# Kernel tuning notes

Hardware: AMD Instinct MI355X
Metric: run time of the kernel (lower is better)

## Reference

```python
import jax, jax.numpy as jnp
import numpy as np

V, H, B, NS, SL, QL, AL = 100000, 256, 64, 40, 30, 20, 12
NUM_EPISODE = 3


def setup_inputs() -> dict:
    key = jax.random.key(0)
    ks = iter(jax.random.split(key, 48))
    def p(shape, scale=0.05):
        return jax.random.normal(next(ks), shape, jnp.float32) * scale
    d = {}
    d["c_p"] = jax.random.randint(next(ks), (B, NS, SL), 0, V, dtype=jnp.int32)
    d["c_mask"] = jnp.zeros((B, NS, SL), jnp.int32)
    d["q_p"] = jax.random.randint(next(ks), (B, QL), 0, V, dtype=jnp.int32)
    d["q_mask"] = jnp.zeros((B, QL), jnp.int32)
    d["a_I_p"] = jax.random.randint(next(ks), (B, AL), 0, V, dtype=jnp.int32)
    d["a_I_mask"] = jnp.zeros((B, AL), jnp.int32)
    d["a_II_p"] = jax.random.randint(next(ks), (B, AL), 0, V, dtype=jnp.int32)
    d["a_II_mask"] = jnp.zeros((B, AL), jnp.int32)
    d["embed"] = p((V, H)).at[0].set(0.0)  # padding_idx=0
    for name in ["ctx", "q", "ans", "attn", "mem"]:
        d[name + "_Wih"] = p((3 * H, H))
        d[name + "_Whh"] = p((3 * H, H))
        d[name + "_bih"] = p((3 * H,))
        d[name + "_bhh"] = p((3 * H,))
    d["gate_W1"] = p((H, 7 * H)); d["gate_b1"] = p((H,))
    d["gate_W2"] = p((1, H));     d["gate_b2"] = p((1,))
    d["out_W1"] = p((H, 3 * H)); d["out_b1"] = p((H,))
    d["out_W2"] = p((2, H));     d["out_b2"] = p((2,))
    return d


def _gru_step(h, gi_t, Whh, bhh):
    # PyTorch GRU cell math; gates ordered (r, z, n)
    gh = h @ Whh.T + bhh
    i_r, i_z, i_n = jnp.split(gi_t, 3, -1)
    h_r, h_z, h_n = jnp.split(gh, 3, -1)
    r = jax.nn.sigmoid(i_r + h_r)
    z = jax.nn.sigmoid(i_z + h_z)
    n = jnp.tanh(i_n + r * h_n)
    return (1.0 - z) * n + z * h


def _run_gru(x, Wih, Whh, bih, bhh):
    # x: [N, T, H] -> outputs [N, T, H], zero initial hidden
    gi = jnp.einsum('nth,gh->ntg', x, Wih) + bih  # precompute input projections
    h0 = jnp.zeros((x.shape[0], Whh.shape[1]), x.dtype)
    def step(h, g_t):
        h2 = _gru_step(h, g_t, Whh, bhh)
        return h2, h2
    _, outs = jax.lax.scan(step, h0, jnp.swapaxes(gi, 0, 1))
    return jnp.swapaxes(outs, 0, 1)


def _gather_last(outs, mask):
    # real_length = number of zeros in mask (0 marks a valid token)
    lengths = jnp.sum(mask == 0, axis=-1)
    idx = jnp.clip(lengths - 1, 0, outs.shape[1] - 1)
    return jnp.take_along_axis(outs, idx[:, None, None], axis=1)[:, 0]


def _forward(c_p, c_mask, q_p, q_mask, a_I_p, a_I_mask, a_II_p, a_II_mask,
             embed,
             ctx_Wih, ctx_Whh, ctx_bih, ctx_bhh,
             q_Wih, q_Whh, q_bih, q_bhh,
             ans_Wih, ans_Whh, ans_bih, ans_bhh,
             attn_Wih, attn_Whh, attn_bih, attn_bhh,
             mem_Wih, mem_Whh, mem_bih, mem_bhh,
             gate_W1, gate_b1, gate_W2, gate_b2,
             out_W1, out_b1, out_W2, out_b2):
    b, ns, sl = c_p.shape
    # Context encoding: all (batch, sentence) pairs through one batched GRU
    ce = embed[c_p.reshape(b * ns, sl)]                      # [B*NS, SL, H]
    c_out = _run_gru(ce, ctx_Wih, ctx_Whh, ctx_bih, ctx_bhh)
    enc_ctx = _gather_last(c_out, c_mask.reshape(b * ns, sl)).reshape(b, ns, -1)  # [B, NS, H]
    # Question / answers
    enc_q = _gather_last(_run_gru(embed[q_p], q_Wih, q_Whh, q_bih, q_bhh), q_mask)          # [B, H]
    enc_a1 = _gather_last(_run_gru(embed[a_I_p], ans_Wih, ans_Whh, ans_bih, ans_bhh), a_I_mask)
    enc_a2 = _gather_last(_run_gru(embed[a_II_p], ans_Wih, ans_Whh, ans_bih, ans_bhh), a_II_mask)
    # Episodic memory: gated attention GRU scan over context sentences
    ctx_t = jnp.swapaxes(enc_ctx, 0, 1)  # [NS, B, H]
    memory = enc_q
    for _ in range(NUM_EPISODE):
        mem_now = memory
        def step(h, ct):
            feat = jnp.concatenate([ct, mem_now, enc_q, ct * enc_q, ct * mem_now,
                                    jnp.abs(ct - enc_q), jnp.abs(ct - mem_now)], axis=1)  # [B, 7H]
            g = jax.nn.sigmoid(jnp.tanh(feat @ gate_W1.T + gate_b1) @ gate_W2.T + gate_b2)  # [B, 1]
            hc = _gru_step(h, ct @ attn_Wih.T + attn_bih, attn_Whh, attn_bhh)
            return g * hc + (1.0 - g) * h, None
        e, _ = jax.lax.scan(step, jnp.zeros_like(memory), ctx_t)
        memory = _gru_step(memory, e @ mem_Wih.T + mem_bih, mem_Whh, mem_bhh)
    final = jnp.concatenate([memory, enc_a1, enc_a2], axis=1)  # [B, 3H]
    logits = jnp.tanh(final @ out_W1.T + out_b1) @ out_W2.T + out_b2  # [B, 2]
    return jax.nn.softmax(logits, axis=-1)


def reference(c_p, c_mask, q_p, q_mask, a_I_p, a_I_mask, a_II_p, a_II_mask,
              embed,
              ctx_Wih, ctx_Whh, ctx_bih, ctx_bhh,
              q_Wih, q_Whh, q_bih, q_bhh,
              ans_Wih, ans_Whh, ans_bih, ans_bhh,
              attn_Wih, attn_Whh, attn_bih, attn_bhh,
              mem_Wih, mem_Whh, mem_bih, mem_bhh,
              gate_W1, gate_b1, gate_W2, gate_b2,
              out_W1, out_b1, out_W2, out_b2):
    return _forward(c_p, c_mask, q_p, q_mask, a_I_p, a_I_mask, a_II_p, a_II_mask,
                    embed,
                    ctx_Wih, ctx_Whh, ctx_bih, ctx_bhh,
                    q_Wih, q_Whh, q_bih, q_bhh,
                    ans_Wih, ans_Whh, ans_bih, ans_bhh,
                    attn_Wih, attn_Whh, attn_bih, attn_bhh,
                    mem_Wih, mem_Whh, mem_bih, mem_bhh,
                    gate_W1, gate_b1, gate_W2, gate_b2,
                    out_W1, out_b1, out_W2, out_b2)
```

## Files before the change

### kernel.cpp

```cpp
#include <hip/hip_runtime.h>

typedef unsigned short u16;
typedef __bf16 bf16x8 __attribute__((ext_vector_type(8)));
typedef float f32x4 __attribute__((ext_vector_type(4)));

#define NSENT 40
#define SLEN 30
#define QLEN 20
#define ALEN 12
#define SCTX 2560

__device__ __forceinline__ float b2f(u16 u){ union{float f; unsigned i;} v; v.i = ((unsigned)u)<<16; return v.f; }
__device__ __forceinline__ u16 f2b(float f){ union{float f; unsigned u;} v; v.f=f; unsigned u=v.u; u += ((u>>16)&1u) + 0x7fffu; return (u16)(u>>16); }
__device__ __forceinline__ float sigm(float x){ return __builtin_amdgcn_rcpf(1.f + __expf(-x)); }
__device__ __forceinline__ float tanh_(float x){
  float a = fminf(fmaxf(2.f*x, -30.f), 30.f);
  float e = __expf(a);
  return 1.f - 2.f*__builtin_amdgcn_rcpf(e + 1.f);
}
__device__ __forceinline__ f32x4 mfma16(bf16x8 a, bf16x8 b, f32x4 c){
  return __builtin_amdgcn_mfma_f32_16x16x32_bf16(a, b, c, 0, 0, 0);
}

__global__ void k_prep(
    const float* cWih, const float* cWhh, const float* qWih, const float* qWhh,
    const float* aWih, const float* aWhh, const float* tWih, const float* tWhh,
    const float* mWih, const float* mWhh, const float* gW1,
    const float* cbih, const float* cbhh, const float* qbih, const float* qbhh,
    const float* abih, const float* abhh, const float* tbih, const float* tbhh,
    u16* P0,u16* P1,u16* P2,u16* P3,u16* P4,u16* P5,u16* P6,u16* P7,
    u16* PmWih, u16* PmWhh, u16* PgW1,
    float* B0,float* B1,float* B2,float* B3,float* B4,float* B5,float* B6,float* B7)
{
  int i = blockIdx.x*512 + threadIdx.x;
  if (i < 1572864){
    int seg = i/196608; int e = i - seg*196608;
    int np = e>>8, k = e&255;
    int g16 = np/48, rem = np - g16*48, gate = rem>>4, cc = rem&15;
    int j = gate*256 + g16*16 + cc;
    const float* S;
    u16* D;
    switch(seg){
      case 0: S=cWih; D=P0; break; case 1: S=cWhh; D=P1; break;
      case 2: S=qWih; D=P2; break; case 3: S=qWhh; D=P3; break;
      case 4: S=aWih; D=P4; break; case 5: S=aWhh; D=P5; break;
      case 6: S=tWih; D=P6; break; default: S=tWhh; D=P7; break;
    }
    D[e] = f2b(S[j*256 + k]);
  } else if (i < 1966080){
    int e = i - 1572864;
    if (e < 196608) PmWih[e]=f2b(mWih[e]);
    else PmWhh[e-196608]=f2b(mWhh[e-196608]);
  } else if (i < 2424832){
    int e = i - 1966080;
    PgW1[e] = f2b(gW1[e]);
  } else {
    int e = i - 2424832;
    int seg = e/768; int np = e - seg*768;
    int g16 = np/48, rem = np - g16*48, gate = rem>>4, cc = rem&15;
    int j = gate*256 + g16*16 + cc;
    const float* S; float* D;
    switch(seg){
      case 0: S=cbih; D=B0; break; case 1: S=cbhh; D=B1; break;
      case 2: S=qbih; D=B2; break; case 3: S=qbhh; D=B3; break;
      case 4: S=abih; D=B4; break; case 5: S=abhh; D=B5; break;
      case 6: S=tbih; D=B6; break; default: S=tbhh; D=B7; break;
    }
    D[np] = S[j];
  }
}

__global__ __launch_bounds__(512, 2) void k_xproj(
    const int* c_p, const int* q_p, const int* a1p, const int* a2p,
    const float* embed,
    const u16* cWihP, const u16* qWihP, const u16* aWihP,
    const float* cBih, const float* qBih, const float* aBih,
    u16* gi_c, u16* gi_q, u16* gi_a1, u16* gi_a2)
{
  __shared__ u16 xb[32][264];
  __shared__ u16 go[32][776];
  int bid=blockIdx.x, tid=threadIdx.x;
  const int* toks; const u16* W; const float* bias; u16* out; int rl;
  if (bid < 2400){ toks=c_p; W=cWihP; bias=cBih; out=gi_c; rl=bid*32; }
  else if (bid < 2440){ toks=q_p; W=qWihP; bias=qBih; out=gi_q; rl=(bid-2400)*32; }
  else if (bid < 2464){ toks=a1p; W=aWihP; bias=aBih; out=gi_a1; rl=(bid-2440)*32; }
  else               { toks=a2p; W=aWihP; bias=aBih; out=gi_a2; rl=(bid-2464)*32; }
  #pragma unroll
  for (int p=0;p<4;p++){
    int i=p*512+tid; int row=i>>6, f4=i&63;
    int tok = toks[rl+row];
    float4 v = *((const float4*)(embed + (long)tok*256) + f4);
    u16* dst = &xb[row][f4*4];
    dst[0]=f2b(v.x); dst[1]=f2b(v.y); dst[2]=f2b(v.z); dst[3]=f2b(v.w);
  }
  const int w=tid>>6, lane=tid&63, c=lane&15, quad=lane>>4;
  f32x4 acc[2][6];
  #pragma unroll
  for (int Mt=0;Mt<2;Mt++)
    #pragma unroll
    for (int nt=0;nt<6;nt++) acc[Mt][nt]=(f32x4){0.f,0.f,0.f,0.f};
  __syncthreads();
  #pragma unroll
  for (int Kt=0;Kt<8;Kt++){
    bf16x8 a0 = *(const bf16x8*)&xb[c][Kt*32+quad*8];
    bf16x8 a1 = *(const bf16x8*)&xb[16+c][Kt*32+quad*8];
    #pragma unroll
    for (int nt=0;nt<6;nt++){
      bf16x8 bfr = *(const bf16x8*)(cWihP==W||qWihP==W||aWihP==W ?
                    W + ((w*6+nt)*16+c)*256 + Kt*32 + quad*8 :
                    W + ((w*6+nt)*16+c)*256 + Kt*32 + quad*8);
      acc[0][nt]=mfma16(a0,bfr,acc[0][nt]);
      acc[1][nt]=mfma16(a1,bfr,acc[1][nt]);
    }
  }
  float biasv[6];
  #pragma unroll
  for (int nt=0;nt<6;nt++) biasv[nt]=bias[(w*6+nt)*16+c];
  #pragma unroll
  for (int Mt=0;Mt<2;Mt++)
    #pragma unroll
    for (int nt=0;nt<6;nt++)
      #pragma unroll
      for (int r=0;r<4;r++)
        go[Mt*16+quad*4+r][(w*6+nt)*16+c]=f2b(acc[Mt][nt][r]+biasv[nt]);
  __syncthreads();
  #pragma unroll
  for (int p=0;p<6;p++){
    int idx=p*512+tid;
    int row=idx/96, ch=idx-row*96;
    *(uint4*)(out + (long)(rl+row)*768 + ch*8) = *(uint4*)((char*)&go[row][0] + ch*16);
  }
}

__global__ __launch_bounds__(512, 2) void k_enc_scan(
    const int* c_mask, const int* q_mask, const int* a1m, const int* a2m,
    const u16* cWhhP, const u16* qWhhP, const u16* aWhhP,
    const float* cBhh, const float* qBhh, const float* aBhh,
    const u16* gi_c, const u16* gi_q, const u16* gi_a1, const u16* gi_a2,
    u16* enc_hi, u16* enc_lo, float* enc_qf, float* enc_a1f, float* enc_a2f)
{
  __shared__ u16 hhi[16][264];
  __shared__ u16 hlo[16][264];
  __shared__ u16 gib[2][16][768];
  __shared__ int idxs[16];
  int bid=blockIdx.x, tid=threadIdx.x;
  const int* msk; const u16* W; const float* bhh; const u16* gi; int T, seq0, mode;
  u16 *ohi=0, *olo=0; float* of=0;
  if (bid<160){ msk=c_mask; W=cWhhP; bhh=cBhh; gi=gi_c; T=SLEN; seq0=bid*16; mode=0; ohi=enc_hi; olo=enc_lo; }
  else if (bid<164){ msk=q_mask; W=qWhhP; bhh=qBhh; gi=gi_q; T=QLEN; seq0=(bid-160)*16; mode=1; of=enc_qf; }
  else if (bid<168){ msk=a1m; W=aWhhP; bhh=aBhh; gi=gi_a1; T=ALEN; seq0=(bid-164)*16; mode=1; of=enc_a1f; }
  else             { msk=a2m; W=aWhhP; bhh=aBhh; gi=gi_a2; T=ALEN; seq0=(bid-168)*16; mode=1; of=enc_a2f; }
  if (tid<16){
    int len=0; const int* mr=msk+(seq0+tid)*T;
    for (int t=0;t<T;t++) len += (mr[t]==0);
    int id=len-1; if(id<0)id=0; if(id>T-1)id=T-1; idxs[tid]=id;
  }
  for (int i=tid;i<16*264;i+=512){ ((u16*)hhi)[i]=0; ((u16*)hlo)[i]=0; }
  const int w=tid>>6, lane=tid&63, c=lane&15, quad=lane>>4;
  float biasv[6];
  #pragma unroll
  for (int nt=0;nt<6;nt++) biasv[nt]=bhh[w*96+nt*16+c];
  uint4 breg[48];
  #pragma unroll
  for (int nt=0;nt<6;nt++)
    #pragma unroll
    for (int Kt=0;Kt<8;Kt++)
      breg[nt*8+Kt] = *(const uint4*)(W + (w*96+nt*16+c)*256 + Kt*32 + quad*8);
  float hreg[8];
  #pragma unroll
  for (int i=0;i<8;i++) hreg[i]=0.f;
  const u16* gp[3];
  #pragma unroll
  for (int p=0;p<3;p++){
    int idx=p*512+tid; int row=idx/96, ch=idx-row*96;
    gp[p] = gi + ((long)(seq0+row)*T)*768 + ch*8;
  }
  u16* gf0 = &gib[0][0][0];
  u16* gf1 = &gib[1][0][0];
  {
    uint4 s0[3];
    #pragma unroll
    for (int p=0;p<3;p++) s0[p]=*(const uint4*)(gp[p]);
    #pragma unroll
    for (int p=0;p<3;p++) *(uint4*)(gf0 + (p*512+tid)*8) = s0[p];
  }
  __syncthreads();
  int cbuf=0;
  for (int t=0;t<T;t++){
    uint4 pre[3];
    bool pf = (t+1<T);
    if (pf){
      #pragma unroll
      for (int p=0;p<3;p++) pre[p]=*(const uint4*)(gp[p]+(long)(t+1)*768);
    }
    f32x4 acc[6];
    #pragma unroll
    for (int nt=0;nt<6;nt++) acc[nt]=(f32x4){0.f,0.f,0.f,0.f};
    #pragma unroll
    for (int Kt=0;Kt<8;Kt++){
      bf16x8 a=*(const bf16x8*)&hhi[c][Kt*32+quad*8];
      #pragma unroll
      for (int nt=0;nt<6;nt++) acc[nt]=mfma16(a,*(const bf16x8*)&breg[nt*8+Kt],acc[nt]);
    }
    #pragma unroll
    for (int Kt=0;Kt<8;Kt++){
      bf16x8 a=*(const bf16x8*)&hlo[c][Kt*32+quad*8];
      #pragma unroll
      for (int nt=0;nt<6;nt++) acc[nt]=mfma16(a,*(const bf16x8*)&breg[nt*8+Kt],acc[nt]);
    }
    if (pf){
      u16* gs = cbuf ? gf0 : gf1;
      #pragma unroll
      for (int p=0;p<3;p++) *(uint4*)(gs + (p*512+tid)*8) = pre[p];
    }
    const u16* gb = cbuf ? gf1 : gf0;
    #pragma unroll
    for (int r=0;r<4;r++){
      int m = quad*4+r;
      const u16* gr = gb + m*768 + w*96 + c;
      #pragma unroll
      for (int jj=0;jj<2;jj++){
        int j = w*32+jj*16+c;
        float ir = b2f(gr[jj*48]);
        float iz = b2f(gr[jj*48+16]);
        float in_= b2f(gr[jj*48+32]);
        float hr = acc[jj*3+0][r]+biasv[jj*3+0];
        float hz = acc[jj*3+1][r]+biasv[jj*3+1];
        float hn = acc[jj*3+2][r]+biasv[jj*3+2];
        float rr=sigm(ir+hr), zz=sigm(iz+hz), nn=tanh_(in_+rr*hn);
        float ho=hreg[r*2+jj];
        float hnew=(1.f-zz)*nn+zz*ho;
        hreg[r*2+jj]=hnew;
        u16 hi_=f2b(hnew); u16 lo_=f2b(hnew-b2f(hi_));
        hhi[m][j]=hi_; hlo[m][j]=lo_;
        if (t==idxs[m]){
          long o=(long)(seq0+m)*256+j;
          if (mode==0){ ohi[o]=hi_; olo[o]=lo_; }
          else of[o]=hnew;
        }
      }
    }
    __syncthreads();
    cbuf^=1;
  }
}

__global__ __launch_bounds__(512, 2) void k_gi(
    const u16* enc_hi, const u16* enc_lo, const u16* tWihP, const float* tBih,
    float* gi_attn, const float* enc_qf, float* mem_f)
{
  int bid=blockIdx.x, tid=threadIdx.x;
  if (bid==40){ for (int i=tid;i<64*256;i+=512) mem_f[i]=enc_qf[i]; return; }
  __shared__ u16 ahi[64][264];
  __shared__ u16 alo[64][264];
  int seq0=bid*64;
  #pragma unroll
  for (int p=0;p<4;p++){
    int i=p*512+tid; int row=i>>5, ch=i&31;
    *(uint4*)((char*)&ahi[row][0]+ch*16) = *((const uint4*)(enc_hi+(long)(seq0+row)*256)+ch);
    *(uint4*)((char*)&alo[row][0]+ch*16) = *((const uint4*)(enc_lo+(long)(seq0+row)*256)+ch);
  }
  const int w=tid>>6, lane=tid&63, c=lane&15, quad=lane>>4;
  f32x4 acc[4][6];
  #pragma unroll
  for (int Mt=0;Mt<4;Mt++)
    #pragma unroll
    for (int nt=0;nt<6;nt++) acc[Mt][nt]=(f32x4){0.f,0.f,0.f,0.f};
  __syncthreads();
  #pragma unroll
  for (int Kt=0;Kt<8;Kt++){
    bf16x8 a[4];
    #pragma unroll
    for (int Mt=0;Mt<4;Mt++) a[Mt]=*(const bf16x8*)&ahi[Mt*16+c][Kt*32+quad*8];
    #pragma unroll
    for (int nt=0;nt<6;nt++){
      bf16x8 bfr=*(const bf16x8*)(tWihP + ((w*6+nt)*16+c)*256 + Kt*32 + quad*8);
      #pragma unroll
      for (int Mt=0;Mt<4;Mt++) acc[Mt][nt]=mfma16(a[Mt],bfr,acc[Mt][nt]);
    }
  }
  #pragma unroll
  for (int Kt=0;Kt<8;Kt++){
    bf16x8 a[4];
    #pragma unroll
    for (int Mt=0;Mt<4;Mt++) a[Mt]=*(const bf16x8*)&alo[Mt*16+c][Kt*32+quad*8];
    #pragma unroll
    for (int nt=0;nt<6;nt++){
      bf16x8 bfr=*(const bf16x8*)(tWihP + ((w*6+nt)*16+c)*256 + Kt*32 + quad*8);
      #pragma unroll
      for (int Mt=0;Mt<4;Mt++) acc[Mt][nt]=mfma16(a[Mt],bfr,acc[Mt][nt]);
    }
  }
  #pragma unroll
  for (int nt=0;nt<6;nt++){
    float bv=tBih[(w*6+nt)*16+c];
    #pragma unroll
    for (int Mt=0;Mt<4;Mt++)
      #pragma unroll
      for (int r=0;r<4;r++)
        gi_attn[(long)(seq0+Mt*16+quad*4+r)*768 + (w*6+nt)*16+c] = acc[Mt][nt][r]+bv;
  }
}

__global__ __launch_bounds__(512, 1) void k_gatepre(
    const u16* enc_hi, const u16* enc_lo, const float* enc_qf,
    const u16* W1, const float* b1, float* partial)
{
  __shared__ float ctf[32][257];
  __shared__ float qvf[32][257];
  __shared__ u16 ab[32][264];
  int bid=blockIdx.x, tid=threadIdx.x, seq0=bid*32;
  #pragma unroll
  for (int p=0;p<16;p++){
    int i=p*512+tid; int row=i>>8, j=i&255;
    int grow=seq0+row; int b=grow/NSENT;
    ctf[row][j]=b2f(enc_hi[(long)grow*256+j])+b2f(enc_lo[(long)grow*256+j]);
    qvf[row][j]=enc_qf[b*256+j];
  }
  const int w=tid>>6, lane=tid&63, c=lane&15, quad=lane>>4;
  f32x4 acc[2][2];
  #pragma unroll
  for (int nt=0;nt<2;nt++){
    float bv=b1[(w*2+nt)*16+c];
// ... 103 lines not shown
    for (int nt=0;nt<2;nt++) s += tanh_(acc[Mt][nt][r])*w2v[nt];
    pm[i]=s;
  }
  #pragma unroll
  for (int off=1;off<16;off<<=1)
    #pragma unroll
    for (int i=0;i<8;i++) pm[i]+=__shfl_xor(pm[i],off,64);
  if (c==0){
    #pragma unroll
    for (int i=0;i<8;i++){ int m=(i>>2)*16+quad*4+(i&3); pl[m][w]=pm[i]; }
  }
  __syncthreads();
  if (tid<32){
    float s=b2v[0];
    #pragma unroll
    for (int ww=0;ww<8;ww++) s+=pl[tid][ww];
    g[seq0+tid]=sigm(s);
  }
}

__global__ __launch_bounds__(512, 2) void k_scan(
    const u16* tWhhP, const float* tBhh,
    const float* gi_attn, const float* g,
    float* mem_f, const u16* mWihB, const u16* mWhhB,
    const float* mbih, const float* mbhh)
{
  __shared__ u16 hb[16][264];
  __shared__ u16 mhi[16][264];
  __shared__ u16 mlo[16][264];
  __shared__ float gia[2][3072];
  __shared__ float gl[4][40];
  __shared__ float gh[4][772];
  __shared__ float gh2[4][772];
  __shared__ float memfl[4][256];
  int bid=blockIdx.x, tid=threadIdx.x, b0=bid*4;
  const int w=tid>>6, lane=tid&63, c=lane&15, quad=lane>>4;
  for (int i=tid;i<16*264;i+=512){ ((u16*)hb)[i]=0; ((u16*)mhi)[i]=0; ((u16*)mlo)[i]=0; }
  for (int i=tid;i<1024;i+=512){
    int m=i>>8, j=i&255;
    float v=mem_f[(b0+m)*256+j]; memfl[m][j]=v;
    u16 hi_=f2b(v); mhi[m][j]=hi_; mlo[m][j]=f2b(v-b2f(hi_));
  }
  if (tid<160){ int m=tid/40, s=tid-m*40; gl[m][s]=g[(b0+m)*40+s]; }
  float biasv[6];
  #pragma unroll
  for (int nt=0;nt<6;nt++) biasv[nt]=tBhh[w*96+nt*16+c];
  uint4 breg[48];
  #pragma unroll
  for (int nt=0;nt<6;nt++)
    #pragma unroll
    for (int Kt=0;Kt<8;Kt++)
      breg[nt*8+Kt] = *(const uint4*)(tWhhP + (w*96+nt*16+c)*256 + Kt*32 + quad*8);
  float hreg[8];
  #pragma unroll
  for (int i=0;i<8;i++) hreg[i]=0.f;
  int i4a = tid, i4b = 512+tid;
  int ma = i4a/192, ca=(i4a-ma*192)*4;
  int mb = i4b/192, cb=(i4b-mb*192)*4;
  const float* gpa = gi_attn + ((long)(b0+ma)*40)*768 + ca;
  const float* gpb = gi_attn + ((long)(b0+mb)*40)*768 + cb;
  {
    float4 v0=*(const float4*)(gpa);
    *(float4*)&gia[0][i4a*4]=v0;
    if (tid<256){ float4 v1=*(const float4*)(gpb); *(float4*)&gia[0][i4b*4]=v1; }
  }
  __syncthreads();
  int cbuf=0;
  for (int s=0;s<NSENT;s++){
    float4 p0, p1;
    bool pf=(s+1<NSENT);
    if (pf){
      p0=*(const float4*)(gpa + (long)(s+1)*768);
      if (tid<256) p1=*(const float4*)(gpb + (long)(s+1)*768);
    }
    f32x4 acc[6];
    #pragma unroll
    for (int nt=0;nt<6;nt++) acc[nt]=(f32x4){0.f,0.f,0.f,0.f};
    #pragma unroll
    for (int Kt=0;Kt<8;Kt++){
      bf16x8 a=*(const bf16x8*)&hb[c][Kt*32+quad*8];
      #pragma unroll
      for (int nt=0;nt<6;nt++) acc[nt]=mfma16(a,*(const bf16x8*)&breg[nt*8+Kt],acc[nt]);
    }
    if (pf){
      float* gs=&gia[1^cbuf][0];
      *(float4*)(gs+i4a*4)=p0;
      if (tid<256) *(float4*)(gs+i4b*4)=p1;
    }
    if (quad==0){
      const float* ga=&gia[cbuf][0];
      #pragma unroll
      for (int r=0;r<4;r++){
        float gv = gl[r][s];
        const float* gr = ga + r*768 + w*96 + c;
        #pragma unroll
        for (int jj=0;jj<2;jj++){
          int j = w*32+jj*16+c;
          float ir = gr[jj*48];
          float iz = gr[jj*48+16];
          float in_= gr[jj*48+32];
          float hr = acc[jj*3+0][r]+biasv[jj*3+0];
          float hz = acc[jj*3+1][r]+biasv[jj*3+1];
          float hn = acc[jj*3+2][r]+biasv[jj*3+2];
          float rr=sigm(ir+hr), zz=sigm(iz+hz), nn=tanh_(in_+rr*hn);
          float ho=hreg[r*2+jj];
          float hc=(1.f-zz)*nn+zz*ho;
          float hnew=gv*hc+(1.f-gv)*ho;
          hreg[r*2+jj]=hnew;
          hb[r][j]=f2b(hnew);
        }
      }
    }
    __syncthreads();
    cbuf^=1;
  }
  f32x4 ai[6], ah[6];
  #pragma unroll
  for (int nt=0;nt<6;nt++){ ai[nt]=(f32x4){0.f,0.f,0.f,0.f}; ah[nt]=ai[nt]; }
  #pragma unroll
  for (int Kt=0;Kt<8;Kt++){
    bf16x8 a=*(const bf16x8*)&hb[c][Kt*32+quad*8];
    #pragma unroll
    for (int nt=0;nt<6;nt++){
      bf16x8 bfr=*(const bf16x8*)(mWihB + ((w*6+nt)*16+c)*256 + Kt*32 + quad*8);
      ai[nt]=mfma16(a,bfr,ai[nt]);
    }
  }
  #pragma unroll
  for (int Kt=0;Kt<8;Kt++){
    bf16x8 a=*(const bf16x8*)&mhi[c][Kt*32+quad*8];
    #pragma unroll
    for (int nt=0;nt<6;nt++){
      bf16x8 bfr=*(const bf16x8*)(mWhhB + ((w*6+nt)*16+c)*256 + Kt*32 + quad*8);
      ah[nt]=mfma16(a,bfr,ah[nt]);
    }
  }
  #pragma unroll
  for (int Kt=0;Kt<8;Kt++){
    bf16x8 a=*(const bf16x8*)&mlo[c][Kt*32+quad*8];
    #pragma unroll
    for (int nt=0;nt<6;nt++){
      bf16x8 bfr=*(const bf16x8*)(mWhhB + ((w*6+nt)*16+c)*256 + Kt*32 + quad*8);
      ah[nt]=mfma16(a,bfr,ah[nt]);
    }
  }
  if (quad==0){
    #pragma unroll
    for (int nt=0;nt<6;nt++)
      #pragma unroll
      for (int r=0;r<4;r++){
        gh[r][(w*6+nt)*16+c]=ai[nt][r];
        gh2[r][(w*6+nt)*16+c]=ah[nt][r];
      }
  }
  __syncthreads();
  #pragma unroll
  for (int p=0;p<2;p++){
    int uid=p*512+tid; int m=uid>>8, j=uid&255;
    float ir=gh[m][j]+mbih[j], iz=gh[m][256+j]+mbih[256+j], in_=gh[m][512+j]+mbih[512+j];
    float hr=gh2[m][j]+mbhh[j], hz=gh2[m][256+j]+mbhh[256+j], hn=gh2[m][512+j]+mbhh[512+j];
    float rr=sigm(ir+hr), zz=sigm(iz+hz), nn=tanh_(in_+rr*hn);
    float mo=memfl[m][j];
    mem_f[(b0+m)*256+j]=(1.f-zz)*nn+zz*mo;
  }
}

__global__ void k_final(const float* mem_f, const float* a1f, const float* a2f,
    const float* W1o, const float* b1o, const float* W2o, const float* b2o, float* outp)
{
  __shared__ float af[768];
  __shared__ float tl[256];
  __shared__ float lg[2];
  int b=blockIdx.x, tid=threadIdx.x;
  af[tid]     = mem_f[b*256+tid];
  af[256+tid] = a1f[b*256+tid];
  af[512+tid] = a2f[b*256+tid];
  __syncthreads();
  float s=b1o[tid];
  const float* wr=W1o + (long)tid*768;
  for (int k=0;k<768;k++) s += af[k]*wr[k];
  tl[tid]=tanh_(s);
  __syncthreads();
  if (tid<2){
    float l=b2o[tid];
    const float* w2=W2o + tid*256;
    for (int k=0;k<256;k++) l += tl[k]*w2[k];
// ... 10 lines not shown

extern "C" void kernel_launch(void* const* d_in, const int* in_sizes, int n_in,
                              void* d_out, int out_size, void* d_ws, size_t ws_size,
                              hipStream_t stream) {
  const int* c_p   = (const int*)d_in[0];
  const int* c_m   = (const int*)d_in[1];
  const int* q_p   = (const int*)d_in[2];
  const int* q_m   = (const int*)d_in[3];
  const int* a1p   = (const int*)d_in[4];
  const int* a1m   = (const int*)d_in[5];
  const int* a2p   = (const int*)d_in[6];
  const int* a2m   = (const int*)d_in[7];
  const float* embed = (const float*)d_in[8];
  const float* cWih=(const float*)d_in[9],  *cWhh=(const float*)d_in[10], *cbih=(const float*)d_in[11], *cbhh=(const float*)d_in[12];
  const float* qWih=(const float*)d_in[13], *qWhh=(const float*)d_in[14], *qbih=(const float*)d_in[15], *qbhh=(const float*)d_in[16];
  const float* aWih=(const float*)d_in[17], *aWhh=(const float*)d_in[18], *abih=(const float*)d_in[19], *abhh=(const float*)d_in[20];
  const float* tWih=(const float*)d_in[21], *tWhh=(const float*)d_in[22], *tbih=(const float*)d_in[23], *tbhh=(const float*)d_in[24];
  const float* mWih=(const float*)d_in[25], *mWhh=(const float*)d_in[26], *mbih=(const float*)d_in[27], *mbhh=(const float*)d_in[28];
  const float* gW1=(const float*)d_in[29], *gb1=(const float*)d_in[30], *gW2=(const float*)d_in[31], *gb2=(const float*)d_in[32];
  const float* oW1=(const float*)d_in[33], *ob1=(const float*)d_in[34], *oW2=(const float*)d_in[35], *ob2=(const float*)d_in[36];

  char* ws = (char*)d_ws;
  size_t off = 0;
  u16* P0=(u16*)(ws+off); off+=393216;
  u16* P1=(u16*)(ws+off); off+=393216;
  u16* P2=(u16*)(ws+off); off+=393216;
  u16* P3=(u16*)(ws+off); off+=393216;
  u16* P4=(u16*)(ws+off); off+=393216;
  u16* P5=(u16*)(ws+off); off+=393216;
  u16* P6=(u16*)(ws+off); off+=393216;
  u16* P7=(u16*)(ws+off); off+=393216;
  u16* PmWih=(u16*)(ws+off); off+=393216;
  u16* PmWhh=(u16*)(ws+off); off+=393216;
  u16* PgW1 =(u16*)(ws+off); off+=917504;
  float* B0=(float*)(ws+off); off+=3072;
  float* B1=(float*)(ws+off); off+=3072;
  float* B2=(float*)(ws+off); off+=3072;
  float* B3=(float*)(ws+off); off+=3072;
  float* B4=(float*)(ws+off); off+=3072;
  float* B5=(float*)(ws+off); off+=3072;
  float* B6=(float*)(ws+off); off+=3072;
  float* B7=(float*)(ws+off); off+=3072;
  u16* gi_c =(u16*)(ws+off); off+=(size_t)76800*768*2;
  u16* gi_q =(u16*)(ws+off); off+=(size_t)1280*768*2;
  u16* gi_a1=(u16*)(ws+off); off+=(size_t)768*768*2;
  u16* gi_a2=(u16*)(ws+off); off+=(size_t)768*768*2;
  u16* enc_hi=(u16*)(ws+off); off+=(size_t)SCTX*256*2;
  u16* enc_lo=(u16*)(ws+off); off+=(size_t)SCTX*256*2;
  float* enc_qf =(float*)(ws+off); off+=64*256*4;
  float* enc_a1f=(float*)(ws+off); off+=64*256*4;
  float* enc_a2f=(float*)(ws+off); off+=64*256*4;
  float* mem_f  =(float*)(ws+off); off+=64*256*4;
  float* gi_attn=(float*)(ws+off); off+=(size_t)SCTX*768*4;
  float* partial=(float*)(ws+off); off+=(size_t)SCTX*256*4;
  float* gbuf   =(float*)(ws+off); off+=SCTX*4;

  k_prep<<<4748, 512, 0, stream>>>(cWih,cWhh,qWih,qWhh,aWih,aWhh,tWih,tWhh,mWih,mWhh,gW1,
      cbih,cbhh,qbih,qbhh,abih,abhh,tbih,tbhh,
      P0,P1,P2,P3,P4,P5,P6,P7, PmWih,PmWhh,PgW1,
      B0,B1,B2,B3,B4,B5,B6,B7);

  k_xproj<<<2488, 512, 0, stream>>>(c_p,q_p,a1p,a2p, embed,
      P0,P2,P4, B0,B2,B4, gi_c,gi_q,gi_a1,gi_a2);

  k_enc_scan<<<172, 512, 0, stream>>>(c_m,q_m,a1m,a2m,
      P1,P3,P5, B1,B3,B5, gi_c,gi_q,gi_a1,gi_a2,
      enc_hi,enc_lo, enc_qf,enc_a1f,enc_a2f);

  k_gi<<<41, 512, 0, stream>>>(enc_hi,enc_lo, P6, B6, gi_attn, enc_qf, mem_f);

  k_gatepre<<<80, 512, 0, stream>>>(enc_hi,enc_lo, enc_qf, PgW1, gb1, partial);

  for (int ep=0; ep<3; ep++){
    k_gate<<<80, 512, 0, stream>>>(enc_hi,enc_lo, mem_f, partial, PgW1, gW2, gb2, gbuf);
    k_scan<<<16, 512, 0, stream>>>(P7, B7, gi_attn, gbuf, mem_f, PmWih, PmWhh, mbih, mbhh);
  }

  k_final<<<64, 256, 0, stream>>>(mem_f, enc_a1f, enc_a2f, oW1, ob1, oW2, ob2, (float*)d_out);
}
```

Before: 957.7 us.

## Store gate projections in per-lane fragment layout and widen attention scan tiles

The input-projection kernels now write gi in a per-lane fragment order (24 values per lane per timestep), and the scans read each lane's slice straight into registers with a register double-buffer. This removes the LDS staging buffers and an extra sync pass. The attention scan now processes 16 batch rows per block in 4 blocks instead of 4 rows in 16, so every MFMA row carries real data. The memory GRU epilogue is done in registers using permuted mem weights. The cost is that only 4 blocks run the serial attention scan, which lowers parallelism.

```diff
diff --git a/kernel.cpp b/kernel.cpp
--- a/kernel.cpp
+++ b/kernel.cpp
@@ -9,6 +9,8 @@
 #define QLEN 20
 #define ALEN 12
 #define SCTX 2560
+#define SLOT 24
+#define TP 12288
 
 __device__ __forceinline__ float b2f(u16 u){ union{float f; unsigned i;} v; v.i = ((unsigned)u)<<16; return v.f; }
 __device__ __forceinline__ u16 f2b(float f){ union{float f; unsigned u;} v; v.f=f; unsigned u=v.u; u += ((u>>16)&1u) + 0x7fffu; return (u16)(u>>16); }
@@ -28,29 +30,27 @@
     const float* mWih, const float* mWhh, const float* gW1,
     const float* cbih, const float* cbhh, const float* qbih, const float* qbhh,
     const float* abih, const float* abhh, const float* tbih, const float* tbhh,
-    u16* P0,u16* P1,u16* P2,u16* P3,u16* P4,u16* P5,u16* P6,u16* P7,
-    u16* PmWih, u16* PmWhh, u16* PgW1,
-    float* B0,float* B1,float* B2,float* B3,float* B4,float* B5,float* B6,float* B7)
+    const float* mbih, const float* mbhh,
+    u16* P0,u16* P1,u16* P2,u16* P3,u16* P4,u16* P5,u16* P6,u16* P7,u16* P8,u16* P9,
+    u16* PgW1,
+    float* B0,float* B1,float* B2,float* B3,float* B4,float* B5,float* B6,float* B7,
+    float* B8,float* B9)
 {
   int i = blockIdx.x*512 + threadIdx.x;
-  if (i < 1572864){
+  if (i < 1966080){
     int seg = i/196608; int e = i - seg*196608;
     int np = e>>8, k = e&255;
     int g16 = np/48, rem = np - g16*48, gate = rem>>4, cc = rem&15;
     int j = gate*256 + g16*16 + cc;
-    const float* S;
-    u16* D;
+    const float* S; u16* D;
     switch(seg){
       case 0: S=cWih; D=P0; break; case 1: S=cWhh; D=P1; break;
       case 2: S=qWih; D=P2; break; case 3: S=qWhh; D=P3; break;
       case 4: S=aWih; D=P4; break; case 5: S=aWhh; D=P5; break;
-      case 6: S=tWih; D=P6; break; default: S=tWhh; D=P7; break;
+      case 6: S=tWih; D=P6; break; case 7: S=tWhh; D=P7; break;
+      case 8: S=mWih; D=P8; break; default: S=mWhh; D=P9; break;
     }
     D[e] = f2b(S[j*256 + k]);
-  } else if (i < 1966080){
-    int e = i - 1572864;
-    if (e < 196608) PmWih[e]=f2b(mWih[e]);
-    else PmWhh[e-196608]=f2b(mWhh[e-196608]);
   } else if (i < 2424832){
     int e = i - 1966080;
     PgW1[e] = f2b(gW1[e]);
@@ -64,7 +64,8 @@
       case 0: S=cbih; D=B0; break; case 1: S=cbhh; D=B1; break;
       case 2: S=qbih; D=B2; break; case 3: S=qbhh; D=B3; break;
       case 4: S=abih; D=B4; break; case 5: S=abhh; D=B5; break;
-      case 6: S=tbih; D=B6; break; default: S=tbhh; D=B7; break;
+      case 6: S=tbih; D=B6; break; case 7: S=tbhh; D=B7; break;
+      case 8: S=mbih; D=B8; break; default: S=mbhh; D=B9; break;
     }
     D[np] = S[j];
   }
@@ -78,17 +79,18 @@
     u16* gi_c, u16* gi_q, u16* gi_a1, u16* gi_a2)
 {
   __shared__ u16 xb[32][264];
-  __shared__ u16 go[32][776];
   int bid=blockIdx.x, tid=threadIdx.x;
-  const int* toks; const u16* W; const float* bias; u16* out; int rl;
-  if (bid < 2400){ toks=c_p; W=cWihP; bias=cBih; out=gi_c; rl=bid*32; }
-  else if (bid < 2440){ toks=q_p; W=qWihP; bias=qBih; out=gi_q; rl=(bid-2400)*32; }
-  else if (bid < 2464){ toks=a1p; W=aWihP; bias=aBih; out=gi_a1; rl=(bid-2440)*32; }
-  else               { toks=a2p; W=aWihP; bias=aBih; out=gi_a2; rl=(bid-2464)*32; }
+  const int* toks; const u16* W; const float* bias; u16* out; int T, block, t0;
+  if (bid < 2400){ toks=c_p; W=cWihP; bias=cBih; out=gi_c; T=SLEN; block=bid/15; t0=(bid-block*15)*2; }
+  else if (bid < 2440){ int e=bid-2400; toks=q_p; W=qWihP; bias=qBih; out=gi_q; T=QLEN; block=e/10; t0=(e-block*10)*2; }
+  else if (bid < 2464){ int e=bid-2440; toks=a1p; W=aWihP; bias=aBih; out=gi_a1; T=ALEN; block=e/6; t0=(e-block*6)*2; }
+  else               { int e=bid-2464; toks=a2p; W=aWihP; bias=aBih; out=gi_a2; T=ALEN; block=e/6; t0=(e-block*6)*2; }
+  int seq0 = block*16;
   #pragma unroll
   for (int p=0;p<4;p++){
     int i=p*512+tid; int row=i>>6, f4=i&63;
-    int tok = toks[rl+row];
+    int tp=row>>4, m=row&15;
+    int tok = toks[(seq0+m)*T + t0+tp];
     float4 v = *((const float4*)(embed + (long)tok*256) + f4);
     u16* dst = &xb[row][f4*4];
     dst[0]=f2b(v.x); dst[1]=f2b(v.y); dst[2]=f2b(v.z); dst[3]=f2b(v.w);
@@ -106,29 +108,30 @@
     bf16x8 a1 = *(const bf16x8*)&xb[16+c][Kt*32+quad*8];
     #pragma unroll
     for (int nt=0;nt<6;nt++){
-      bf16x8 bfr = *(const bf16x8*)(cWihP==W||qWihP==W||aWihP==W ?
-                    W + ((w*6+nt)*16+c)*256 + Kt*32 + quad*8 :
-                    W + ((w*6+nt)*16+c)*256 + Kt*32 + quad*8);
+      bf16x8 bfr = *(const bf16x8*)(W + (w*96+nt*16+c)*256 + Kt*32 + quad*8);
       acc[0][nt]=mfma16(a0,bfr,acc[0][nt]);
       acc[1][nt]=mfma16(a1,bfr,acc[1][nt]);
     }
   }
   float biasv[6];
   #pragma unroll
-  for (int nt=0;nt<6;nt++) biasv[nt]=bias[(w*6+nt)*16+c];
-  #pragma unroll
-  for (int Mt=0;Mt<2;Mt++)
-    #pragma unroll
-    for (int nt=0;nt<6;nt++)
-      #pragma unroll
-      for (int r=0;r<4;r++)
-        go[Mt*16+quad*4+r][(w*6+nt)*16+c]=f2b(acc[Mt][nt][r]+biasv[nt]);
-  __syncthreads();
-  #pragma unroll
-  for (int p=0;p<6;p++){
-    int idx=p*512+tid;
-    int row=idx/96, ch=idx-row*96;
-    *(uint4*)(out + (long)(rl+row)*768 + ch*8) = *(uint4*)((char*)&go[row][0] + ch*16);
+  for (int nt=0;nt<6;nt++) biasv[nt]=bias[w*96+nt*16+c];
+  #pragma unroll
+  for (int tp=0;tp<2;tp++){
+    unsigned d[12];
+    #pragma unroll
+    for (int k=0;k<12;k++){
+      int i0=2*k, i1=2*k+1;
+      int r0=i0/6, re0=i0%6, jj0=re0/3, g0=re0%3;
+      int r1=i1/6, re1=i1%6, jj1=re1/3, g1=re1%3;
+      unsigned lo=f2b(acc[tp][jj0*3+g0][r0]+biasv[jj0*3+g0]);
+      unsigned hi=f2b(acc[tp][jj1*3+g1][r1]+biasv[jj1*3+g1]);
+      d[k] = lo | (hi<<16);
+    }
+    u16* dst = out + ((long)(block*T + t0+tp))*TP + (w*64+lane)*SLOT;
+    *(uint4*)(dst)    = *(uint4*)&d[0];
+    *(uint4*)(dst+8)  = *(uint4*)&d[4];
+    *(uint4*)(dst+16) = *(uint4*)&d[8];
   }
 }
 
@@ -141,15 +144,14 @@
 {
   __shared__ u16 hhi[16][264];
   __shared__ u16 hlo[16][264];
-  __shared__ u16 gib[2][16][768];
   __shared__ int idxs[16];
   int bid=blockIdx.x, tid=threadIdx.x;
   const int* msk; const u16* W; const float* bhh; const u16* gi; int T, seq0, mode;
   u16 *ohi=0, *olo=0; float* of=0;
-  if (bid<160){ msk=c_mask; W=cWhhP; bhh=cBhh; gi=gi_c; T=SLEN; seq0=bid*16; mode=0; ohi=enc_hi; olo=enc_lo; }
-  else if (bid<164){ msk=q_mask; W=qWhhP; bhh=qBhh; gi=gi_q; T=QLEN; seq0=(bid-160)*16; mode=1; of=enc_qf; }
-  else if (bid<168){ msk=a1m; W=aWhhP; bhh=aBhh; gi=gi_a1; T=ALEN; seq0=(bid-164)*16; mode=1; of=enc_a1f; }
-  else             { msk=a2m; W=aWhhP; bhh=aBhh; gi=gi_a2; T=ALEN; seq0=(bid-168)*16; mode=1; of=enc_a2f; }
+  if (bid<160){ msk=c_mask; W=cWhhP; bhh=cBhh; gi=gi_c+(long)bid*SLEN*TP; T=SLEN; seq0=bid*16; mode=0; ohi=enc_hi; olo=enc_lo; }
+  else if (bid<164){ int e=bid-160; msk=q_mask; W=qWhhP; bhh=qBhh; gi=gi_q+(long)e*QLEN*TP; T=QLEN; seq0=e*16; mode=1; of=enc_qf; }
+  else if (bid<168){ int e=bid-164; msk=a1m; W=aWhhP; bhh=aBhh; gi=gi_a1+(long)e*ALEN*TP; T=ALEN; seq0=e*16; mode=1; of=enc_a1f; }
+  else             { int e=bid-168; msk=a2m; W=aWhhP; bhh=aBhh; gi=gi_a2+(long)e*ALEN*TP; T=ALEN; seq0=e*16; mode=1; of=enc_a2f; }
   if (tid<16){
     int len=0; const int* mr=msk+(seq0+tid)*T;
     for (int t=0;t<T;t++) len += (mr[t]==0);
@@ -169,29 +171,19 @@
   float hreg[8];
   #pragma unroll
   for (int i=0;i<8;i++) hreg[i]=0.f;
-  const u16* gp[3];
-  #pragma unroll
-  for (int p=0;p<3;p++){
-    int idx=p*512+tid; int row=idx/96, ch=idx-row*96;
-    gp[p] = gi + ((long)(seq0+row)*T)*768 + ch*8;
-  }
-  u16* gf0 = &gib[0][0][0];
-  u16* gf1 = &gib[1][0][0];
-  {
-    uint4 s0[3];
-    #pragma unroll
-    for (int p=0;p<3;p++) s0[p]=*(const uint4*)(gp[p]);
-    #pragma unroll
-    for (int p=0;p<3;p++) *(uint4*)(gf0 + (p*512+tid)*8) = s0[p];
-  }
-  __syncthreads();
-  int cbuf=0;
+  const u16* gp = gi + (w*64+lane)*SLOT;
+  uint4 pA0=*(const uint4*)(gp), pA1=*(const uint4*)(gp+8), pA2=*(const uint4*)(gp+16);
+  __syncthreads();
+  int idxr[4];
+  #pragma unroll
+  for (int r=0;r<4;r++) idxr[r]=idxs[quad*4+r];
+
   for (int t=0;t<T;t++){
-    uint4 pre[3];
-    bool pf = (t+1<T);
+    uint4 pB0,pB1,pB2;
+    bool pf=(t+1<T);
     if (pf){
-      #pragma unroll
-      for (int p=0;p<3;p++) pre[p]=*(const uint4*)(gp[p]+(long)(t+1)*768);
+      const u16* gn = gp + (long)(t+1)*TP;
+      pB0=*(const uint4*)(gn); pB1=*(const uint4*)(gn+8); pB2=*(const uint4*)(gn+16);
     }
     f32x4 acc[6];
     #pragma unroll
@@ -208,32 +200,28 @@
       #pragma unroll
       for (int nt=0;nt<6;nt++) acc[nt]=mfma16(a,*(const bf16x8*)&breg[nt*8+Kt],acc[nt]);
     }
-    if (pf){
-      u16* gs = cbuf ? gf0 : gf1;
-      #pragma unroll
-      for (int p=0;p<3;p++) *(uint4*)(gs + (p*512+tid)*8) = pre[p];
-    }
-    const u16* gb = cbuf ? gf1 : gf0;
+    unsigned pd[12];
+    *(uint4*)&pd[0]=pA0; *(uint4*)&pd[4]=pA1; *(uint4*)&pd[8]=pA2;
     #pragma unroll
     for (int r=0;r<4;r++){
-      int m = quad*4+r;
-      const u16* gr = gb + m*768 + w*96 + c;
+      int m=quad*4+r;
       #pragma unroll
       for (int jj=0;jj<2;jj++){
-        int j = w*32+jj*16+c;
-        float ir = b2f(gr[jj*48]);
-        float iz = b2f(gr[jj*48+16]);
-        float in_= b2f(gr[jj*48+32]);
-        float hr = acc[jj*3+0][r]+biasv[jj*3+0];
-        float hz = acc[jj*3+1][r]+biasv[jj*3+1];
-        float hn = acc[jj*3+2][r]+biasv[jj*3+2];
+        int j=w*32+jj*16+c;
+        int ib=(r*2+jj)*3;
+        float ir = b2f((u16)((pd[ib>>1]     >> ((ib&1)*16)) & 0xffffu));
+        float iz = b2f((u16)((pd[(ib+1)>>1] >> (((ib+1)&1)*16)) & 0xffffu));
+        float in_= b2f((u16)((pd[(ib+2)>>1] >> (((ib+2)&1)*16)) & 0xffffu));
+        float hr=acc[jj*3+0][r]+biasv[jj*3+0];
+        float hz=acc[jj*3+1][r]+biasv[jj*3+1];
+        float hn=acc[jj*3+2][r]+biasv[jj*3+2];
         float rr=sigm(ir+hr), zz=sigm(iz+hz), nn=tanh_(in_+rr*hn);
         float ho=hreg[r*2+jj];
         float hnew=(1.f-zz)*nn+zz*ho;
         hreg[r*2+jj]=hnew;
         u16 hi_=f2b(hnew); u16 lo_=f2b(hnew-b2f(hi_));
         hhi[m][j]=hi_; hlo[m][j]=lo_;
-        if (t==idxs[m]){
+        if (t==idxr[r]){
           long o=(long)(seq0+m)*256+j;
           if (mode==0){ ohi[o]=hi_; olo[o]=lo_; }
           else of[o]=hnew;
@@ -241,7 +229,7 @@
       }
     }
     __syncthreads();
-    cbuf^=1;
+    pA0=pB0; pA1=pB1; pA2=pB2;
   }
 }
 
@@ -250,55 +238,53 @@
     float* gi_attn, const float* enc_qf, float* mem_f)
 {
   int bid=blockIdx.x, tid=threadIdx.x;
-  if (bid==40){ for (int i=tid;i<64*256;i+=512) mem_f[i]=enc_qf[i]; return; }
-  __shared__ u16 ahi[64][264];
-  __shared__ u16 alo[64][264];
-  int seq0=bid*64;
-  #pragma unroll
-  for (int p=0;p<4;p++){
-    int i=p*512+tid; int row=i>>5, ch=i&31;
-    *(uint4*)((char*)&ahi[row][0]+ch*16) = *((const uint4*)(enc_hi+(long)(seq0+row)*256)+ch);
-    *(uint4*)((char*)&alo[row][0]+ch*16) = *((const uint4*)(enc_lo+(long)(seq0+row)*256)+ch);
+  if (bid==160){ for (int i=tid;i<64*256;i+=512) mem_f[i]=enc_qf[i]; return; }
+  __shared__ u16 ahi[16][264];
+  __shared__ u16 alo[16][264];
+  int bblk=bid/40, s=bid-bblk*40, b0=bblk*16;
+  {
+    int row=tid>>5, ch=tid&31;
+    long seq=(long)(b0+row)*NSENT + s;
+    *(uint4*)((char*)&ahi[row][0]+ch*16) = *((const uint4*)(enc_hi+seq*256)+ch);
+    *(uint4*)((char*)&alo[row][0]+ch*16) = *((const uint4*)(enc_lo+seq*256)+ch);
   }
   const int w=tid>>6, lane=tid&63, c=lane&15, quad=lane>>4;
-  f32x4 acc[4][6];
-  #pragma unroll
-  for (int Mt=0;Mt<4;Mt++)
-    #pragma unroll
-    for (int nt=0;nt<6;nt++) acc[Mt][nt]=(f32x4){0.f,0.f,0.f,0.f};
+  f32x4 acc[6];
+  #pragma unroll
+  for (int nt=0;nt<6;nt++) acc[nt]=(f32x4){0.f,0.f,0.f,0.f};
   __syncthreads();
   #pragma unroll
   for (int Kt=0;Kt<8;Kt++){
-    bf16x8 a[4];
-    #pragma unroll
-    for (int Mt=0;Mt<4;Mt++) a[Mt]=*(const bf16x8*)&ahi[Mt*16+c][Kt*32+quad*8];
+    bf16x8 a=*(const bf16x8*)&ahi[c][Kt*32+quad*8];
     #pragma unroll
     for (int nt=0;nt<6;nt++){
-      bf16x8 bfr=*(const bf16x8*)(tWihP + ((w*6+nt)*16+c)*256 + Kt*32 + quad*8);
-      #pragma unroll
-      for (int Mt=0;Mt<4;Mt++) acc[Mt][nt]=mfma16(a[Mt],bfr,acc[Mt][nt]);
+      bf16x8 bfr=*(const bf16x8*)(tWihP + (w*96+nt*16+c)*256 + Kt*32 + quad*8);
+      acc[nt]=mfma16(a,bfr,acc[nt]);
     }
   }
   #pragma unroll
   for (int Kt=0;Kt<8;Kt++){
-    bf16x8 a[4];
-    #pragma unroll
-    for (int Mt=0;Mt<4;Mt++) a[Mt]=*(const bf16x8*)&alo[Mt*16+c][Kt*32+quad*8];
+    bf16x8 a=*(const bf16x8*)&alo[c][Kt*32+quad*8];
     #pragma unroll
     for (int nt=0;nt<6;nt++){
-      bf16x8 bfr=*(const bf16x8*)(tWihP + ((w*6+nt)*16+c)*256 + Kt*32 + quad*8);
-      #pragma unroll
-      for (int Mt=0;Mt<4;Mt++) acc[Mt][nt]=mfma16(a[Mt],bfr,acc[Mt][nt]);
-    }
-  }
-  #pragma unroll
-  for (int nt=0;nt<6;nt++){
-    float bv=tBih[(w*6+nt)*16+c];
-    #pragma unroll
-    for (int Mt=0;Mt<4;Mt++)
-      #pragma unroll
-      for (int r=0;r<4;r++)
-        gi_attn[(long)(seq0+Mt*16+quad*4+r)*768 + (w*6+nt)*16+c] = acc[Mt][nt][r]+bv;
+      bf16x8 bfr=*(const bf16x8*)(tWihP + (w*96+nt*16+c)*256 + Kt*32 + quad*8);
+      acc[nt]=mfma16(a,bfr,acc[nt]);
+    }
+  }
+  float biasv[6];
+  #pragma unroll
+  for (int nt=0;nt<6;nt++) biasv[nt]=tBih[w*96+nt*16+c];
+  float* dst = gi_attn + ((long)(bblk*40+s))*TP + (w*64+lane)*SLOT;
+  #pragma unroll
+  for (int d=0;d<6;d++){
+    float4 v;
+    #pragma unroll
+    for (int e=0;e<4;e++){
+      int idx=4*d+e;
+      int r=idx/6, rem=idx%6, jj=rem/3, g=rem%3;
+      ((float*)&v)[e]=acc[jj*3+g][r]+biasv[jj*3+g];
+    }
+    *(float4*)(dst+4*d)=v;
   }
 }
 
@@ -448,26 +434,23 @@
 __global__ __launch_bounds__(512, 2) void k_scan(
     const u16* tWhhP, const float* tBhh,
     const float* gi_attn, const float* g,
-    float* mem_f, const u16* mWihB, const u16* mWhhB,
-    const float* mbih, const float* mbhh)
+    float* mem_f, const u16* mWihP, const u16* mWhhP,
+    const float* mBih, const float* mBhh)
 {
   __shared__ u16 hb[16][264];
   __shared__ u16 mhi[16][264];
   __shared__ u16 mlo[16][264];
-  __shared__ float gia[2][3072];
-  __shared__ float gl[4][40];
-  __shared__ float gh[4][772];
-  __shared__ float gh2[4][772];
-  __shared__ float memfl[4][256];
-  int bid=blockIdx.x, tid=threadIdx.x, b0=bid*4;
+  __shared__ float memfl[16][256];
+  __shared__ float gl[16][40];
+  int bid=blockIdx.x, tid=threadIdx.x, b0=bid*16;
   const int w=tid>>6, lane=tid&63, c=lane&15, quad=lane>>4;
-  for (int i=tid;i<16*264;i+=512){ ((u16*)hb)[i]=0; ((u16*)mhi)[i]=0; ((u16*)mlo)[i]=0; }
-  for (int i=tid;i<1024;i+=512){
+  for (int i=tid;i<16*264;i+=512){ ((u16*)hb)[i]=0; }
+  for (int i=tid;i<4096;i+=512){
     int m=i>>8, j=i&255;
     float v=mem_f[(b0+m)*256+j]; memfl[m][j]=v;
     u16 hi_=f2b(v); mhi[m][j]=hi_; mlo[m][j]=f2b(v-b2f(hi_));
   }
-  if (tid<160){ int m=tid/40, s=tid-m*40; gl[m][s]=g[(b0+m)*40+s]; }
+  for (int i=tid;i<640;i+=512){ int m=i/40, s=i-m*40; gl[m][s]=g[(b0+m)*40+s]; }
   float biasv[6];
   #pragma unroll
   for (int nt=0;nt<6;nt++) biasv[nt]=tBhh[w*96+nt*16+c];
@@ -480,24 +463,19 @@
   float hreg[8];
   #pragma unroll
   for (int i=0;i<8;i++) hreg[i]=0.f;
-  int i4a = tid, i4b = 512+tid;
-  int ma = i4a/192, ca=(i4a-ma*192)*4;
-  int mb = i4b/192, cb=(i4b-mb*192)*4;
-  const float* gpa = gi_attn + ((long)(b0+ma)*40)*768 + ca;
-  const float* gpb = gi_attn + ((long)(b0+mb)*40)*768 + cb;
-  {
-    float4 v0=*(const float4*)(gpa);
-    *(float4*)&gia[0][i4a*4]=v0;
-    if (tid<256){ float4 v1=*(const float4*)(gpb); *(float4*)&gia[0][i4b*4]=v1; }
-  }
-  __syncthreads();
-  int cbuf=0;
+  const float* gp = gi_attn + ((long)bid*NSENT)*TP + (w*64+lane)*SLOT;
+  float4 pA[6];
+  #pragma unroll
+  for (int d=0;d<6;d++) pA[d]=*(const float4*)(gp+4*d);
+  __syncthreads();
+
   for (int s=0;s<NSENT;s++){
-    float4 p0, p1;
+    float4 pB[6];
     bool pf=(s+1<NSENT);
     if (pf){
-      p0=*(const float4*)(gpa + (long)(s+1)*768);
-      if (tid<256) p1=*(const float4*)(gpb + (long)(s+1)*768);
+      const float* gn = gp + (long)(s+1)*TP;
+      #pragma unroll
+      for (int d=0;d<6;d++) pB[d]=*(const float4*)(gn+4*d);
     }
     f32x4 acc[6];
     #pragma unroll
@@ -508,37 +486,30 @@
       #pragma unroll
       for (int nt=0;nt<6;nt++) acc[nt]=mfma16(a,*(const bf16x8*)&breg[nt*8+Kt],acc[nt]);
     }
-    if (pf){
-      float* gs=&gia[1^cbuf][0];
-      *(float4*)(gs+i4a*4)=p0;
-      if (tid<256) *(float4*)(gs+i4b*4)=p1;
-    }
-    if (quad==0){
-      const float* ga=&gia[cbuf][0];
-      #pragma unroll
-      for (int r=0;r<4;r++){
-        float gv = gl[r][s];
-        const float* gr = ga + r*768 + w*96 + c;
-        #pragma unroll
-        for (int jj=0;jj<2;jj++){
-          int j = w*32+jj*16+c;
-          float ir = gr[jj*48];
-          float iz = gr[jj*48+16];
-          float in_= gr[jj*48+32];
-          float hr = acc[jj*3+0][r]+biasv[jj*3+0];
-          float hz = acc[jj*3+1][r]+biasv[jj*3+1];
-          float hn = acc[jj*3+2][r]+biasv[jj*3+2];
-          float rr=sigm(ir+hr), zz=sigm(iz+hz), nn=tanh_(in_+rr*hn);
-          float ho=hreg[r*2+jj];
-          float hc=(1.f-zz)*nn+zz*ho;
-          float hnew=gv*hc+(1.f-gv)*ho;
-          hreg[r*2+jj]=hnew;
-          hb[r][j]=f2b(hnew);
-        }
+    const float* pf32 = (const float*)&pA[0];
+    #pragma unroll
+    for (int r=0;r<4;r++){
+      int m=quad*4+r;
+      float gv = gl[m][s];
+      #pragma unroll
+      for (int jj=0;jj<2;jj++){
+        int j=w*32+jj*16+c;
+        int ib=(r*2+jj)*3;
+        float ir=pf32[ib], iz=pf32[ib+1], in_=pf32[ib+2];
+        float hr=acc[jj*3+0][r]+biasv[jj*3+0];
+        float hz=acc[jj*3+1][r]+biasv[jj*3+1];
+        float hn=acc[jj*3+2][r]+biasv[jj*3+2];
+        float rr=sigm(ir+hr), zz=sigm(iz+hz), nn=tanh_(in_+rr*hn);
+        float ho=hreg[r*2+jj];
+        float hc=(1.f-zz)*nn+zz*ho;
+        float hnew=gv*hc+(1.f-gv)*ho;
+        hreg[r*2+jj]=hnew;
+        hb[m][j]=f2b(hnew);
       }
     }
     __syncthreads();
-    cbuf^=1;
+    #pragma unroll
+    for (int d=0;d<6;d++) pA[d]=pB[d];
   }
   f32x4 ai[6], ah[6];
   #pragma unroll
@@ -548,7 +519,7 @@
     bf16x8 a=*(const bf16x8*)&hb[c][Kt*32+quad*8];
     #pragma unroll
     for (int nt=0;nt<6;nt++){
-      bf16x8 bfr=*(const bf16x8*)(mWihB + ((w*6+nt)*16+c)*256 + Kt*32 + quad*8);
+      bf16x8 bfr=*(const bf16x8*)(mWihP + (w*96+nt*16+c)*256 + Kt*32 + quad*8);
       ai[nt]=mfma16(a,bfr,ai[nt]);
     }
   }
@@ -557,7 +528,7 @@
     bf16x8 a=*(const bf16x8*)&mhi[c][Kt*32+quad*8];
     #pragma unroll
     for (int nt=0;nt<6;nt++){
-      bf16x8 bfr=*(const bf16x8*)(mWhhB + ((w*6+nt)*16+c)*256 + Kt*32 + quad*8);
+      bf16x8 bfr=*(const bf16x8*)(mWhhP + (w*96+nt*16+c)*256 + Kt*32 + quad*8);
       ah[nt]=mfma16(a,bfr,ah[nt]);
     }
   }
@@ -566,28 +537,29 @@
     bf16x8 a=*(const bf16x8*)&mlo[c][Kt*32+quad*8];
     #pragma unroll
     for (int nt=0;nt<6;nt++){
-      bf16x8 bfr=*(const bf16x8*)(mWhhB + ((w*6+nt)*16+c)*256 + Kt*32 + quad*8);
+      bf16x8 bfr=*(const bf16x8*)(mWhhP + (w*96+nt*16+c)*256 + Kt*32 + quad*8);
       ah[nt]=mfma16(a,bfr,ah[nt]);
     }
   }
-  if (quad==0){
-    #pragma unroll
-    for (int nt=0;nt<6;nt++)
-      #pragma unroll
-      for (int r=0;r<4;r++){
-        gh[r][(w*6+nt)*16+c]=ai[nt][r];
-        gh2[r][(w*6+nt)*16+c]=ah[nt][r];
-      }
-  }
-  __syncthreads();
-  #pragma unroll
-  for (int p=0;p<2;p++){
-    int uid=p*512+tid; int m=uid>>8, j=uid&255;
-    float ir=gh[m][j]+mbih[j], iz=gh[m][256+j]+mbih[256+j], in_=gh[m][512+j]+mbih[512+j];
-    float hr=gh2[m][j]+mbhh[j], hz=gh2[m][256+j]+mbhh[256+j], hn=gh2[m][512+j]+mbhh[512+j];
-    float rr=sigm(ir+hr), zz=sigm(iz+hz), nn=tanh_(in_+rr*hn);
-    float mo=memfl[m][j];
-    mem_f[(b0+m)*256+j]=(1.f-zz)*nn+zz*mo;
+  float bih6[6], bhh6[6];
+  #pragma unroll
+  for (int nt=0;nt<6;nt++){ bih6[nt]=mBih[w*96+nt*16+c]; bhh6[nt]=mBhh[w*96+nt*16+c]; }
+  #pragma unroll
+  for (int r=0;r<4;r++){
+    int m=quad*4+r;
+    #pragma unroll
+    for (int jj=0;jj<2;jj++){
+      int j=w*32+jj*16+c;
+      float ir=ai[jj*3+0][r]+bih6[jj*3+0];
+      float iz=ai[jj*3+1][r]+bih6[jj*3+1];
+      float in_=ai[jj*3+2][r]+bih6[jj*3+2];
+      float hr=ah[jj*3+0][r]+bhh6[jj*3+0];
+      float hz=ah[jj*3+1][r]+bhh6[jj*3+1];
+      float hn=ah[jj*3+2][r]+bhh6[jj*3+2];
+      float rr=sigm(ir+hr), zz=sigm(iz+hz), nn=tanh_(in_+rr*hn);
+      float mo=memfl[m][j];
+      mem_f[(b0+m)*256+j]=(1.f-zz)*nn+zz*mo;
+    }
   }
 }
 
@@ -644,58 +616,44 @@
 
   char* ws = (char*)d_ws;
   size_t off = 0;
-  u16* P0=(u16*)(ws+off); off+=393216;
-  u16* P1=(u16*)(ws+off); off+=393216;
-  u16* P2=(u16*)(ws+off); off+=393216;
-  u16* P3=(u16*)(ws+off); off+=393216;
-  u16* P4=(u16*)(ws+off); off+=393216;
-  u16* P5=(u16*)(ws+off); off+=393216;
-  u16* P6=(u16*)(ws+off); off+=393216;
-  u16* P7=(u16*)(ws+off); off+=393216;
-  u16* PmWih=(u16*)(ws+off); off+=393216;
-  u16* PmWhh=(u16*)(ws+off); off+=393216;
+  u16* P[10];
+  for (int i=0;i<10;i++){ P[i]=(u16*)(ws+off); off+=393216; }
   u16* PgW1 =(u16*)(ws+off); off+=917504;
-  float* B0=(float*)(ws+off); off+=3072;
-  float* B1=(float*)(ws+off); off+=3072;
-  float* B2=(float*)(ws+off); off+=3072;
-  float* B3=(float*)(ws+off); off+=3072;
-  float* B4=(float*)(ws+off); off+=3072;
-  float* B5=(float*)(ws+off); off+=3072;
-  float* B6=(float*)(ws+off); off+=3072;
-  float* B7=(float*)(ws+off); off+=3072;
-  u16* gi_c =(u16*)(ws+off); off+=(size_t)76800*768*2;
-  u16* gi_q =(u16*)(ws+off); off+=(size_t)1280*768*2;
-  u16* gi_a1=(u16*)(ws+off); off+=(size_t)768*768*2;
-  u16* gi_a2=(u16*)(ws+off); off+=(size_t)768*768*2;
+  float* B[10];
+  for (int i=0;i<10;i++){ B[i]=(float*)(ws+off); off+=3072; }
+  u16* gi_c =(u16*)(ws+off); off+=(size_t)160*SLEN*TP*2;
+  u16* gi_q =(u16*)(ws+off); off+=(size_t)4*QLEN*TP*2;
+  u16* gi_a1=(u16*)(ws+off); off+=(size_t)4*ALEN*TP*2;
+  u16* gi_a2=(u16*)(ws+off); off+=(size_t)4*ALEN*TP*2;
   u16* enc_hi=(u16*)(ws+off); off+=(size_t)SCTX*256*2;
   u16* enc_lo=(u16*)(ws+off); off+=(size_t)SCTX*256*2;
   float* enc_qf =(float*)(ws+off); off+=64*256*4;
   float* enc_a1f=(float*)(ws+off); off+=64*256*4;
   float* enc_a2f=(float*)(ws+off); off+=64*256*4;
   float* mem_f  =(float*)(ws+off); off+=64*256*4;
-  float* gi_attn=(float*)(ws+off); off+=(size_t)SCTX*768*4;
+  float* gi_attn=(float*)(ws+off); off+=(size_t)160*TP*4;
   float* partial=(float*)(ws+off); off+=(size_t)SCTX*256*4;
   float* gbuf   =(float*)(ws+off); off+=SCTX*4;
 
-  k_prep<<<4748, 512, 0, stream>>>(cWih,cWhh,qWih,qWhh,aWih,aWhh,tWih,tWhh,mWih,mWhh,gW1,
-      cbih,cbhh,qbih,qbhh,abih,abhh,tbih,tbhh,
-      P0,P1,P2,P3,P4,P5,P6,P7, PmWih,PmWhh,PgW1,
-      B0,B1,B2,B3,B4,B5,B6,B7);
+  k_prep<<<4751, 512, 0, stream>>>(cWih,cWhh,qWih,qWhh,aWih,aWhh,tWih,tWhh,mWih,mWhh,gW1,
+      cbih,cbhh,qbih,qbhh,abih,abhh,tbih,tbhh,mbih,mbhh,
+      P[0],P[1],P[2],P[3],P[4],P[5],P[6],P[7],P[8],P[9], PgW1,
+      B[0],B[1],B[2],B[3],B[4],B[5],B[6],B[7],B[8],B[9]);
 
   k_xproj<<<2488, 512, 0, stream>>>(c_p,q_p,a1p,a2p, embed,
-      P0,P2,P4, B0,B2,B4, gi_c,gi_q,gi_a1,gi_a2);
+      P[0],P[2],P[4], B[0],B[2],B[4], gi_c,gi_q,gi_a1,gi_a2);
 
   k_enc_scan<<<172, 512, 0, stream>>>(c_m,q_m,a1m,a2m,
-      P1,P3,P5, B1,B3,B5, gi_c,gi_q,gi_a1,gi_a2,
+      P[1],P[3],P[5], B[1],B[3],B[5], gi_c,gi_q,gi_a1,gi_a2,
       enc_hi,enc_lo, enc_qf,enc_a1f,enc_a2f);
 
-  k_gi<<<41, 512, 0, stream>>>(enc_hi,enc_lo, P6, B6, gi_attn, enc_qf, mem_f);
+  k_gi<<<161, 512, 0, stream>>>(enc_hi,enc_lo, P[6], B[6], gi_attn, enc_qf, mem_f);
 
   k_gatepre<<<80, 512, 0, stream>>>(enc_hi,enc_lo, enc_qf, PgW1, gb1, partial);
 
   for (int ep=0; ep<3; ep++){
     k_gate<<<80, 512, 0, stream>>>(enc_hi,enc_lo, mem_f, partial, PgW1, gW2, gb2, gbuf);
-    k_scan<<<16, 512, 0, stream>>>(P7, B7, gi_attn, gbuf, mem_f, PmWih, PmWhh, mbih, mbhh);
+    k_scan<<<4, 512, 0, stream>>>(P[7], B[7], gi_attn, gbuf, mem_f, P[8], P[9], B[8], B[9]);
   }
 
   k_final<<<64, 256, 0, stream>>>(mem_f, enc_a1f, enc_a2f, oW1, ob1, oW2, ob2, (float*)d_out);
```

Measured after the change: 934.2 us. 1.03x faster.
